# Optimization experiments

Measured on AMD Instinct MI355X. Metric: run time of the kernel, lower is better.

Reference implementation:

```python
import jax, jax.numpy as jnp
import numpy as np

N_NODES = 100000
N_EDGES = 1600000
N_GRAPHS = 64
D_NODE = 32
D_EDGE = 32
D_U = 32
OUT_DIM = 64
IN1 = 2 * D_NODE + D_EDGE + D_U  # 128
IN2 = D_NODE + OUT_DIM + D_U      # 128


def setup_inputs() -> dict:
    key = jax.random.key(0)
    ks = jax.random.split(key, 9)
    x = jax.random.normal(ks[0], (N_NODES, D_NODE), dtype=jnp.float32)
    edge_index = jax.random.randint(ks[1], (2, N_EDGES), 0, N_NODES, dtype=jnp.int64)
    edge_attr = jax.random.normal(ks[2], (N_EDGES, D_EDGE), dtype=jnp.float32)
    u = jax.random.normal(ks[3], (N_GRAPHS, D_U), dtype=jnp.float32)
    batch = jnp.sort(jax.random.randint(ks[4], (N_NODES,), 0, N_GRAPHS, dtype=jnp.int64))
    W1 = jax.random.normal(ks[5], (IN1, OUT_DIM), dtype=jnp.float32) * (1.0 / np.sqrt(IN1))
    b1 = jax.random.normal(ks[6], (OUT_DIM,), dtype=jnp.float32) * 0.01
    W2 = jax.random.normal(ks[7], (IN2, OUT_DIM), dtype=jnp.float32) * (1.0 / np.sqrt(IN2))
    b2 = jax.random.normal(ks[8], (OUT_DIM,), dtype=jnp.float32) * 0.01
    return {"x": x, "edge_index": edge_index, "edge_attr": edge_attr, "u": u,
            "batch": batch, "W1": W1, "b1": b1, "W2": W2, "b2": b2}


def reference(x, edge_index, edge_attr, u, batch, W1, b1, W2, b2):
    src, dest = edge_index[0], edge_index[1]
    u_node = u[batch]                     # [N_NODES, D_U]
    u_edge = u_node[src]                  # [N_EDGES, D_U] == u[batch][src]
    # Edge-level MLP1: concat gathered features then Linear+ReLU
    m_in = jnp.concatenate([x[dest], x[src], edge_attr, u_edge], axis=-1)
    messages = jax.nn.relu(m_in @ W1 + b1)            # [N_EDGES, OUT_DIM]
    # scatter-sum messages onto destination nodes
    agg = jax.ops.segment_sum(messages, dest, num_segments=x.shape[0])
    # Node-level MLP2
    n_in = jnp.concatenate([x, agg, u_node], axis=-1)  # [N_NODES, IN2]
    return jax.nn.relu(n_in @ W2 + b2)                 # [N_NODES, OUT_DIM]
```

## Files before the change

### kernel.cpp

```cpp
#include <hip/hip_runtime.h>


constexpr int kNodes  = 100000;
constexpr int kEdges  = 1600000;
constexpr int kGraphs = 64;
constexpr int kD      = 32;
constexpr int kOut    = 64;
constexpr int kTiles  = kEdges / 16;
constexpr int SB      = 256;
constexpr int NB      = (kNodes + SB - 1) / SB;
static_assert(kEdges % 16 == 0, "tile-exact");
static_assert(NB <= 512, "scan_top handles <=512 block sums");

using frag_b = __attribute__((ext_vector_type(8))) short;
using f32x4  = __attribute__((ext_vector_type(4))) float;

__device__ __forceinline__ short f2bf(float f) {
  unsigned u = __float_as_uint(f);
  return (short)((u + 0x7FFFu + ((u >> 16) & 1u)) >> 16);
}
__device__ __forceinline__ float bf2f(short h) {
  return __uint_as_float((unsigned)(unsigned short)h << 16);
}

__global__ __launch_bounds__(256) void cvt_kernel(const float* __restrict__ src,
                                                  short* __restrict__ dst,
                                                  int n4) {
  int i = blockIdx.x * 256 + threadIdx.x;
  int stride = gridDim.x * 256;
  for (; i < n4; i += stride) {
    float4 v = reinterpret_cast<const float4*>(src)[i];
    short4 h;
    h.x = f2bf(v.x); h.y = f2bf(v.y); h.z = f2bf(v.z); h.w = f2bf(v.w);
    reinterpret_cast<short4*>(dst)[i] = h;
  }
}

__global__ __launch_bounds__(256) void w1pack_kernel(
    const float* __restrict__ W1, uint4* __restrict__ W1p) {
  int idx = blockIdx.x * 256 + threadIdx.x;
  if (idx >= 1024) return;
  int lane = idx & 63, ntile = (idx >> 6) & 3, ts = idx >> 8;
  int n  = ntile * 16 + (lane & 15);
  int k0 = ts * 32 + ((lane >> 4) & 3) * 8;
  unsigned w[4];
#pragma unroll
  for (int p = 0; p < 4; ++p) {
    unsigned lo = (unsigned short)f2bf(W1[(size_t)(k0 + 2 * p) * kOut + n]);
    unsigned hi = (unsigned short)f2bf(W1[(size_t)(k0 + 2 * p + 1) * kOut + n]);
    w[p] = lo | (hi << 16);
  }
  W1p[idx] = make_uint4(w[0], w[1], w[2], w[3]);
}

__global__ __launch_bounds__(256) void tables_kernel(
    const float* __restrict__ u, const float* __restrict__ W2,
    const float* __restrict__ b2, float* __restrict__ U2) {
  int t = blockIdx.x * 256 + threadIdx.x;
  if (t >= kGraphs * kOut) return;
  int g = t >> 6, j = t & 63;
  float a2 = b2[j];
#pragma unroll
  for (int k = 0; k < kD; ++k)
    a2 = fmaf(u[g * kD + k], W2[(size_t)(96 + k) * kOut + j], a2);
  U2[t] = a2;
}

__global__ __launch_bounds__(256) void hist_kernel(const int* __restrict__ ei,
                                                   int* __restrict__ counts) {
  int i = blockIdx.x * 256 + threadIdx.x;
  int stride = gridDim.x * 256;
  for (int e = i; e < kEdges; e += stride)
    atomicAdd(&counts[ei[kEdges + e]], 1);
}

__global__ __launch_bounds__(SB) void scan_reduce(const int* __restrict__ counts,
                                                  int* __restrict__ bsum) {
  __shared__ int s[SB];
  int i = blockIdx.x * SB + threadIdx.x;
  s[threadIdx.x] = (i < kNodes) ? counts[i] : 0;
  __syncthreads();
  for (int off = SB / 2; off > 0; off >>= 1) {
    if (threadIdx.x < off) s[threadIdx.x] += s[threadIdx.x + off];
    __syncthreads();
  }
  if (threadIdx.x == 0) bsum[blockIdx.x] = s[0];
}

__global__ __launch_bounds__(512) void scan_top(int* __restrict__ bsum) {
  __shared__ int s[512];
  int t = threadIdx.x;
  int orig = (t < NB) ? bsum[t] : 0;
  s[t] = orig;
  __syncthreads();
  for (int off = 1; off < 512; off <<= 1) {
    int a = (t >= off) ? s[t - off] : 0;
    __syncthreads();
    s[t] += a;
    __syncthreads();
  }
  if (t < NB) bsum[t] = s[t] - orig;
}

__global__ __launch_bounds__(SB) void scan_final(
    const int* __restrict__ counts, const int* __restrict__ bscan,
    int* __restrict__ offs, int* __restrict__ cursor) {
  __shared__ int s[SB];
  int i = blockIdx.x * SB + threadIdx.x;
  int v = (i < kNodes) ? counts[i] : 0;
  s[threadIdx.x] = v;
  __syncthreads();
  for (int off = 1; off < SB; off <<= 1) {
    int a = (threadIdx.x >= off) ? s[threadIdx.x - off] : 0;
    __syncthreads();
    s[threadIdx.x] += a;
    __syncthreads();
  }
  if (i < kNodes) {
    int ex = s[threadIdx.x] - v + bscan[blockIdx.x];
    offs[i] = ex;
    cursor[i] = ex;
  }
  if (blockIdx.x == 0 && threadIdx.x == 0) offs[kNodes] = kEdges;
}

__global__ __launch_bounds__(256) void slot_kernel(const int* __restrict__ ei,
                                                   int* __restrict__ cursor,
                                                   int* __restrict__ pos) {
  int i = blockIdx.x * 256 + threadIdx.x;
  int stride = gridDim.x * 256;
  for (int e = i; e < kEdges; e += stride)
    pos[e] = atomicAdd(&cursor[ei[kEdges + e]], 1);
}

__global__ __launch_bounds__(256) void edge_mfma_kernel(
    const int* __restrict__ ei, const int* __restrict__ batch,
    const short* __restrict__ xb, const short* __restrict__ eab,
    const short* __restrict__ ub, const uint4* __restrict__ W1p,
    const float* __restrict__ b1, const int* __restrict__ pos,
    short* __restrict__ msgbuf) {
  __shared__ uint4 sW[1024];
  for (int i = threadIdx.x; i < 1024; i += 256) sW[i] = W1p[i];
  __syncthreads();
  const int lane = threadIdx.x & 63;
  const int er   = lane & 15;
  const int kq   = lane >> 4;
  const int koff = kq * 8;
  float b1v[4];
#pragma unroll
  for (int n = 0; n < 4; ++n) b1v[n] = b1[n * 16 + er];
  const int wave = (blockIdx.x * 256 + threadIdx.x) >> 6;
  const int nw   = gridDim.x * 4;
  for (int t = wave; t < kTiles; t += nw) {
    const int tb = t * 16;
    const int s  = ei[tb + er];
    const int d  = ei[kEdges + tb + er];
    const int g  = batch[s];
    const uint4 pv = *reinterpret_cast<const uint4*>(pos + tb + kq * 4);
    frag_b a0 = *reinterpret_cast<const frag_b*>(xb + (size_t)d * kD + koff);
    frag_b a1 = *reinterpret_cast<const frag_b*>(xb + (size_t)s * kD + koff);
    frag_b a2 =
        *reinterpret_cast<const frag_b*>(eab + (size_t)(tb + er) * kD + koff);
    frag_b a3 = *reinterpret_cast<const frag_b*>(ub + g * kD + koff);
    f32x4 acc[4];
#pragma unroll
    for (int n = 0; n < 4; ++n) {
      acc[n] = (f32x4){0.f, 0.f, 0.f, 0.f};
      acc[n] = __builtin_amdgcn_mfma_f32_16x16x32_bf16(
          a0, *reinterpret_cast<const frag_b*>(&sW[(0 * 4 + n) * 64 + lane]),
          acc[n], 0, 0, 0);
      acc[n] = __builtin_amdgcn_mfma_f32_16x16x32_bf16(
          a1, *reinterpret_cast<const frag_b*>(&sW[(1 * 4 + n) * 64 + lane]),
          acc[n], 0, 0, 0);
      acc[n] = __builtin_amdgcn_mfma_f32_16x16x32_bf16(
          a2, *reinterpret_cast<const frag_b*>(&sW[(2 * 4 + n) * 64 + lane]),
          acc[n], 0, 0, 0);
      acc[n] = __builtin_amdgcn_mfma_f32_16x16x32_bf16(
          a3, *reinterpret_cast<const frag_b*>(&sW[(3 * 4 + n) * 64 + lane]),
          acc[n], 0, 0, 0);
    }
    const int prow[4] = {(int)pv.x, (int)pv.y, (int)pv.z, (int)pv.w};
#pragma unroll
    for (int n = 0; n < 4; ++n)
#pragma unroll
      for (int r = 0; r < 4; ++r) {
        float v = fmaxf(acc[n][r] + b1v[n], 0.f);
        msgbuf[(size_t)prow[r] * kOut + n * 16 + er] = f2bf(v);
      }
  }
}

__global__ __launch_bounds__(256) void sum_mlp2_kernel(
    const float* __restrict__ x, const short* __restrict__ msgbuf,
    const int* __restrict__ offs, const int* __restrict__ batch,
    const float* __restrict__ U2, const float* __restrict__ W2,
    float* __restrict__ out) {
  __shared__ float sWa[kD * kOut];
  __shared__ float sWb[kOut * kOut];
  __shared__ float aggrow[4 * kOut];
  for (int i = threadIdx.x; i < kD * kOut; i += 256) sWa[i] = W2[i];
  for (int i = threadIdx.x; i < kOut * kOut; i += 256)
    sWb[i] = W2[kD * kOut + i];
  __syncthreads();
  const int lane = threadIdx.x & 63;
  const int wv   = threadIdx.x >> 6;
  const int wave = (blockIdx.x * 256 + threadIdx.x) >> 6;
  const int nw   = gridDim.x * 4;
  for (int n = wave; n < kNodes; n += nw) {
    const int rb = offs[n], re = offs[n + 1];
    float a0 = 0.f, a1 = 0.f;
    int r = rb;
    for (; r + 1 < re; r += 2) {
      a0 += bf2f(msgbuf[(size_t)r * kOut + lane]);
      a1 += bf2f(msgbuf[(size_t)(r + 1) * kOut + lane]);
    }
    if (r < re) a0 += bf2f(msgbuf[(size_t)r * kOut + lane]);
    aggrow[wv * kOut + lane] = a0 + a1;
    float acc = U2[batch[n] * kOut + lane];
    const float4* xr = reinterpret_cast<const float4*>(x + (size_t)n * kD);
#pragma unroll
    for (int q = 0; q < 8; ++q) {
      float4 v = xr[q];
      int k = q * 4;
      acc = fmaf(v.x, sWa[(k + 0) * kOut + lane], acc);
      acc = fmaf(v.y, sWa[(k + 1) * kOut + lane], acc);
      acc = fmaf(v.z, sWa[(k + 2) * kOut + lane], acc);
      acc = fmaf(v.w, sWa[(k + 3) * kOut + lane], acc);
    }
#pragma unroll
    for (int q = 0; q < 16; ++q) {
      float4 v = *reinterpret_cast<const float4*>(&aggrow[wv * kOut + q * 4]);
      int k = q * 4;
      acc = fmaf(v.x, sWb[(k + 0) * kOut + lane], acc);
      acc = fmaf(v.y, sWb[(k + 1) * kOut + lane], acc);
      acc = fmaf(v.z, sWb[(k + 2) * kOut + lane], acc);
      acc = fmaf(v.w, sWb[(k + 3) * kOut + lane], acc);
    }
    out[(size_t)n * kOut + lane] = fmaxf(acc, 0.f);
  }
}

extern "C" void kernel_launch(void* const* d_in, const int* in_sizes, int n_in,
                              void* d_out, int out_size, void* d_ws,
                              size_t ws_size, hipStream_t stream) {
  const float* x     = (const float*)d_in[0];
  const int*   ei    = (const int*)d_in[1];
  const float* ea    = (const float*)d_in[2];
  const float* u     = (const float*)d_in[3];
  const int*   batch = (const int*)d_in[4];
  const float* W1    = (const float*)d_in[5];
  const float* b1    = (const float*)d_in[6];
  const float* W2    = (const float*)d_in[7];
  const float* b2    = (const float*)d_in[8];
  float* out = (float*)d_out;

  uint4* W1p   = (uint4*)d_ws;
  float* U2    = (float*)(W1p + 1024);
  int*   counts= (int*)(U2 + kGraphs * kOut);
  int*   offs  = counts + kNodes;
  int*   cursor= offs + kNodes + 1;
  int*   bsum  = cursor + kNodes;
  int*   pos   = bsum + 512;
  short* xb    = (short*)(pos + kEdges);
  short* ub    = xb + (size_t)kNodes * kD;
  short* eab   = ub + kGraphs * kD;
  short* msgbuf= eab + (size_t)kEdges * kD;

  hipMemsetAsync(counts, 0, (size_t)kNodes * sizeof(int), stream);
  cvt_kernel<<<2048, 256, 0, stream>>>(ea, eab, kEdges * kD / 4);
  cvt_kernel<<<512, 256, 0, stream>>>(x, xb, kNodes * kD / 4);
  cvt_kernel<<<2, 256, 0, stream>>>(u, ub, kGraphs * kD / 4);
  w1pack_kernel<<<4, 256, 0, stream>>>(W1, W1p);
  tables_kernel<<<(kGraphs * kOut + 255) / 256, 256, 0, stream>>>(u, W2, b2,
                                                                  U2);
  hist_kernel<<<2048, 256, 0, stream>>>(ei, counts);
  scan_reduce<<<NB, SB, 0, stream>>>(counts, bsum);
  scan_top<<<1, 512, 0, stream>>>(bsum);
  scan_final<<<NB, SB, 0, stream>>>(counts, bsum, offs, cursor);
  slot_kernel<<<2048, 256, 0, stream>>>(ei, cursor, pos);
  edge_mfma_kernel<<<2048, 256, 0, stream>>>(ei, batch, xb, eab, ub, W1p, b1,
                                             pos, msgbuf);
  sum_mlp2_kernel<<<1024, 256, 0, stream>>>(x, msgbuf, offs, batch, U2, W2,
                                            out);
}
```

Before: 840.6 us.

## Fuse edge_attr bf16 conversion into edge kernel and vectorize segment sum reads

Drops the separate pass that converts edge_attr to bf16. The edge MFMA kernel now reads fp32 edge features directly and packs them to bf16 in registers, which avoids writing and re-reading a 102MB intermediate. The per-node segment sum now has each lane read 16-byte chunks covering 8 message rows at once and reduces them with a cross-lane shuffle tree, plus a scalar tail loop. The node kernel grid is doubled and workspace buffers are 256-byte aligned. The cost is more register pressure and some shuffle overhead on nodes with few edges.

```diff
diff --git a/kernel.cpp b/kernel.cpp
--- a/kernel.cpp
+++ b/kernel.cpp
@@ -19,8 +19,18 @@
   unsigned u = __float_as_uint(f);
   return (short)((u + 0x7FFFu + ((u >> 16) & 1u)) >> 16);
 }
+__device__ __forceinline__ unsigned pk2bf(float lo, float hi) {
+  return (unsigned)(unsigned short)f2bf(lo) |
+         ((unsigned)(unsigned short)f2bf(hi) << 16);
+}
 __device__ __forceinline__ float bf2f(short h) {
   return __uint_as_float((unsigned)(unsigned short)h << 16);
+}
+__device__ __forceinline__ float bflo(unsigned w) {
+  return __uint_as_float(w << 16);
+}
+__device__ __forceinline__ float bfhi(unsigned w) {
+  return __uint_as_float(w & 0xFFFF0000u);
 }
 
 __global__ __launch_bounds__(256) void cvt_kernel(const float* __restrict__ src,
@@ -45,11 +55,9 @@
   int k0 = ts * 32 + ((lane >> 4) & 3) * 8;
   unsigned w[4];
 #pragma unroll
-  for (int p = 0; p < 4; ++p) {
-    unsigned lo = (unsigned short)f2bf(W1[(size_t)(k0 + 2 * p) * kOut + n]);
-    unsigned hi = (unsigned short)f2bf(W1[(size_t)(k0 + 2 * p + 1) * kOut + n]);
-    w[p] = lo | (hi << 16);
-  }
+  for (int p = 0; p < 4; ++p)
+    w[p] = pk2bf(W1[(size_t)(k0 + 2 * p) * kOut + n],
+                 W1[(size_t)(k0 + 2 * p + 1) * kOut + n]);
   W1p[idx] = make_uint4(w[0], w[1], w[2], w[3]);
 }
 
@@ -135,7 +143,7 @@
 
 __global__ __launch_bounds__(256) void edge_mfma_kernel(
     const int* __restrict__ ei, const int* __restrict__ batch,
-    const short* __restrict__ xb, const short* __restrict__ eab,
+    const short* __restrict__ xb, const float* __restrict__ ea,
     const short* __restrict__ ub, const uint4* __restrict__ W1p,
     const float* __restrict__ b1, const int* __restrict__ pos,
     short* __restrict__ msgbuf) {
@@ -159,9 +167,15 @@
     const uint4 pv = *reinterpret_cast<const uint4*>(pos + tb + kq * 4);
     frag_b a0 = *reinterpret_cast<const frag_b*>(xb + (size_t)d * kD + koff);
     frag_b a1 = *reinterpret_cast<const frag_b*>(xb + (size_t)s * kD + koff);
-    frag_b a2 =
-        *reinterpret_cast<const frag_b*>(eab + (size_t)(tb + er) * kD + koff);
+    const float4* ef =
+        reinterpret_cast<const float4*>(ea + (size_t)(tb + er) * kD + koff);
+    float4 e0 = ef[0], e1 = ef[1];
     frag_b a3 = *reinterpret_cast<const frag_b*>(ub + g * kD + koff);
+    union { frag_b f; unsigned w[4]; } a2u;
+    a2u.w[0] = pk2bf(e0.x, e0.y);
+    a2u.w[1] = pk2bf(e0.z, e0.w);
+    a2u.w[2] = pk2bf(e1.x, e1.y);
+    a2u.w[3] = pk2bf(e1.z, e1.w);
     f32x4 acc[4];
 #pragma unroll
     for (int n = 0; n < 4; ++n) {
@@ -173,7 +187,7 @@
           a1, *reinterpret_cast<const frag_b*>(&sW[(1 * 4 + n) * 64 + lane]),
           acc[n], 0, 0, 0);
       acc[n] = __builtin_amdgcn_mfma_f32_16x16x32_bf16(
-          a2, *reinterpret_cast<const frag_b*>(&sW[(2 * 4 + n) * 64 + lane]),
+          a2u.f, *reinterpret_cast<const frag_b*>(&sW[(2 * 4 + n) * 64 + lane]),
           acc[n], 0, 0, 0);
       acc[n] = __builtin_amdgcn_mfma_f32_16x16x32_bf16(
           a3, *reinterpret_cast<const frag_b*>(&sW[(3 * 4 + n) * 64 + lane]),
@@ -206,16 +220,29 @@
   const int wv   = threadIdx.x >> 6;
   const int wave = (blockIdx.x * 256 + threadIdx.x) >> 6;
   const int nw   = gridDim.x * 4;
+  const int c0   = (lane & 7) * 8;
   for (int n = wave; n < kNodes; n += nw) {
     const int rb = offs[n], re = offs[n + 1];
-    float a0 = 0.f, a1 = 0.f;
+    float vs[8];
+#pragma unroll
+    for (int j = 0; j < 8; ++j) vs[j] = 0.f;
     int r = rb;
-    for (; r + 1 < re; r += 2) {
-      a0 += bf2f(msgbuf[(size_t)r * kOut + lane]);
-      a1 += bf2f(msgbuf[(size_t)(r + 1) * kOut + lane]);
+    for (; r + 8 <= re; r += 8) {
+      uint4 w = reinterpret_cast<const uint4*>(msgbuf + (size_t)r * kOut)[lane];
+      vs[0] += bflo(w.x); vs[1] += bfhi(w.x);
+      vs[2] += bflo(w.y); vs[3] += bfhi(w.y);
+      vs[4] += bflo(w.z); vs[5] += bfhi(w.z);
+      vs[6] += bflo(w.w); vs[7] += bfhi(w.w);
     }
-    if (r < re) a0 += bf2f(msgbuf[(size_t)r * kOut + lane]);
-    aggrow[wv * kOut + lane] = a0 + a1;
+#pragma unroll
+    for (int st = 8; st < 64; st <<= 1)
+#pragma unroll
+      for (int j = 0; j < 8; ++j) vs[j] += __shfl_xor(vs[j], st);
+#pragma unroll
+    for (int j = 0; j < 8; ++j) aggrow[wv * kOut + c0 + j] = vs[j];
+    float tail = 0.f;
+    for (; r < re; ++r) tail += bf2f(msgbuf[(size_t)r * kOut + lane]);
+    aggrow[wv * kOut + lane] += tail;
     float acc = U2[batch[n] * kOut + lane];
     const float4* xr = reinterpret_cast<const float4*>(x + (size_t)n * kD);
 #pragma unroll
@@ -254,20 +281,22 @@
   const float* b2    = (const float*)d_in[8];
   float* out = (float*)d_out;
 
-  uint4* W1p   = (uint4*)d_ws;
-  float* U2    = (float*)(W1p + 1024);
-  int*   counts= (int*)(U2 + kGraphs * kOut);
-  int*   offs  = counts + kNodes;
-  int*   cursor= offs + kNodes + 1;
-  int*   bsum  = cursor + kNodes;
-  int*   pos   = bsum + 512;
-  short* xb    = (short*)(pos + kEdges);
-  short* ub    = xb + (size_t)kNodes * kD;
-  short* eab   = ub + kGraphs * kD;
-  short* msgbuf= eab + (size_t)kEdges * kD;
+  auto align256 = [](char* p) {
+    return (char*)(((size_t)p + 255) & ~(size_t)255);
+  };
+  char* p = (char*)d_ws;
+  uint4* W1p = (uint4*)p;                 p = align256(p + 1024 * 16);
+  float* U2  = (float*)p;                 p = align256(p + kGraphs * kOut * 4);
+  int* counts = (int*)p;                  p = align256(p + kNodes * 4);
+  int* offs   = (int*)p;                  p = align256(p + (kNodes + 1) * 4);
+  int* cursor = (int*)p;                  p = align256(p + kNodes * 4);
+  int* bsum   = (int*)p;                  p = align256(p + 512 * 4);
+  int* pos    = (int*)p;                  p = align256(p + (size_t)kEdges * 4);
+  short* xb   = (short*)p;                p = align256(p + (size_t)kNodes * kD * 2);
+  short* ub   = (short*)p;                p = align256(p + kGraphs * kD * 2);
+  short* msgbuf = (short*)p;
 
   hipMemsetAsync(counts, 0, (size_t)kNodes * sizeof(int), stream);
-  cvt_kernel<<<2048, 256, 0, stream>>>(ea, eab, kEdges * kD / 4);
   cvt_kernel<<<512, 256, 0, stream>>>(x, xb, kNodes * kD / 4);
   cvt_kernel<<<2, 256, 0, stream>>>(u, ub, kGraphs * kD / 4);
   w1pack_kernel<<<4, 256, 0, stream>>>(W1, W1p);
@@ -278,8 +307,8 @@
   scan_top<<<1, 512, 0, stream>>>(bsum);
   scan_final<<<NB, SB, 0, stream>>>(counts, bsum, offs, cursor);
   slot_kernel<<<2048, 256, 0, stream>>>(ei, cursor, pos);
-  edge_mfma_kernel<<<2048, 256, 0, stream>>>(ei, batch, xb, eab, ub, W1p, b1,
+  edge_mfma_kernel<<<2048, 256, 0, stream>>>(ei, batch, xb, ea, ub, W1p, b1,
                                              pos, msgbuf);
-  sum_mlp2_kernel<<<1024, 256, 0, stream>>>(x, msgbuf, offs, batch, U2, W2,
+  sum_mlp2_kernel<<<2048, 256, 0, stream>>>(x, msgbuf, offs, batch, U2, W2,
                                             out);
 }
```

Result: faster. 767.4 us (-8.7%).
